# Performance work log

Measured on AMD Instinct MI355X. Metric: run time of the kernel, lower is better.

Reference implementation:

```python
import jax, jax.numpy as jnp
import numpy as np

IN_F = 4096      # in_features (d_model)
OUT_F = 16384    # out_features (4*d_model FFN)
N_TOK = 8192     # tokens = batch*seq
K = OUT_F // 2   # number of kept output rows (static for jit)


def setup_inputs() -> dict:
    key = jax.random.key(0)
    k1, k2, k3, k4 = jax.random.split(key, 4)
    data = jax.random.normal(k1, (N_TOK, IN_F), jnp.float32)
    weight = jax.random.normal(k2, (OUT_F, IN_F), jnp.float32) * 0.02
    bias = jax.random.normal(k3, (OUT_F,), jnp.float32) * 0.02
    # mask with exactly K ones at random positions (static count -> jit-safe)
    perm = jax.random.permutation(k4, OUT_F)
    mask = jnp.zeros((OUT_F,), jnp.int32).at[perm[:K]].set(1)
    return {"data": data, "weight": weight, "bias": bias, "mask": mask}


def reference(data, weight, bias, mask):
    # mask.nonzero()[0] -> selected output-feature indices (ascending, as torch)
    idx = jnp.nonzero(mask, size=K)[0]                 # [K]
    w_sel = jnp.take(weight, idx, axis=0)              # [K, IN_F] row gather
    b_sel = jnp.take(bias, idx, axis=0)                # [K]
    # F.linear: data @ w_sel^T + b_sel  -> [N_TOK, K]
    return jnp.einsum('ti,ki->tk', data, w_sel) + b_sel
```

## Files before the change

### kernel.cpp

```cpp
#include <hip/hip_runtime.h>
#include <hip/hip_bf16.h>

typedef __bf16 bf16_t;
typedef __attribute__((ext_vector_type(8))) __bf16 bf16x8;
typedef __attribute__((ext_vector_type(4))) float f32x4;

constexpr int IN_F  = 4096;
constexpr int OUT_F = 16384;
constexpr int N_TOK = 8192;
constexpr int KSEL  = 8192;
constexpr long A_ELEMS = (long)N_TOK * IN_F;

constexpr int BM = 256, BN = 256, BK = 32;
constexpr int NT = IN_F / BK;
constexpr int TILE_E = BM * BK;

#define GLOBAL_CAST(p) (const __attribute__((address_space(1))) void*)(p)
#define LDS_CAST(p)    (__attribute__((address_space(3))) void*)(p)

__global__ __launch_bounds__(1024) void build_idx_kernel(
    const int* __restrict__ mask, const float* __restrict__ bias,
    int* __restrict__ idx, float* __restrict__ bsel)
{
    const int t    = threadIdx.x;
    const int lane = t & 63;
    const int wave = t >> 6;
    const int base_i = t * 16;

    int m[16];
    const int4* mp = (const int4*)(mask + base_i);
#pragma unroll
    for (int v = 0; v < 4; ++v) {
        int4 q = mp[v];
        m[v*4+0] = q.x; m[v*4+1] = q.y; m[v*4+2] = q.z; m[v*4+3] = q.w;
    }
    int cnt = 0;
#pragma unroll
    for (int j = 0; j < 16; ++j) cnt += (m[j] != 0) ? 1 : 0;

    int incl = cnt;
#pragma unroll
    for (int d = 1; d < 64; d <<= 1) {
        int o = __shfl_up(incl, (unsigned)d);
        if (lane >= d) incl += o;
    }

    __shared__ int wsum[16];
    __shared__ int wbase[16];
    if (lane == 63) wsum[wave] = incl;
    __syncthreads();
    if (t == 0) {
        int s = 0;
        for (int w = 0; w < 16; ++w) { wbase[w] = s; s += wsum[w]; }
    }
    __syncthreads();

    int p = wbase[wave] + (incl - cnt);
#pragma unroll
    for (int j = 0; j < 16; ++j) {
        if (m[j]) {
            int i = base_i + j;
            idx[p]  = i;
            bsel[p] = bias[i];
            ++p;
        }
    }
}

__global__ __launch_bounds__(256) void convert_kernel(
    const float* __restrict__ A, const float* __restrict__ W,
    const int* __restrict__ idx,
    bf16_t* __restrict__ Ab, bf16_t* __restrict__ Wb)
{
    const long nvecA = A_ELEMS / 8;
    const long total = nvecA * 2;
    const long stride = (long)gridDim.x * blockDim.x;
    for (long v = (long)blockIdx.x * blockDim.x + threadIdx.x; v < total; v += stride) {
        const float4* src;
        bf16_t* dst;
        if (v < nvecA) {
            src = (const float4*)(A + v * 8);
            dst = Ab + v * 8;
        } else {
            long u = v - nvecA;
            int j = (int)(u >> 9);
            int k = (int)(u & 511) * 8;
            src = (const float4*)(W + (long)idx[j] * IN_F + k);
            dst = Wb + u * 8;
        }
        float4 x = src[0], y = src[1];
        bf16x8 o;
        o[0]=(bf16_t)x.x; o[1]=(bf16_t)x.y; o[2]=(bf16_t)x.z; o[3]=(bf16_t)x.w;
        o[4]=(bf16_t)y.x; o[5]=(bf16_t)y.y; o[6]=(bf16_t)y.z; o[7]=(bf16_t)y.w;
        *(bf16x8*)dst = o;
    }
}

__global__ __launch_bounds__(512, 2) void gemm8_kernel(
    const bf16_t* __restrict__ A, const bf16_t* __restrict__ B,
    const float* __restrict__ bsel, float* __restrict__ C)
{
    __shared__ __attribute__((aligned(16))) bf16_t As[4][TILE_E];
    __shared__ __attribute__((aligned(16))) bf16_t Bs[4][TILE_E];

    const int tid  = threadIdx.x;
    const int w    = tid >> 6;
    const int lane = tid & 63;
    const int wr   = w >> 2;
    const int wc   = w & 3;

    const int bid = blockIdx.x;
    const int swz = (bid & 7) * 128 + (bid >> 3);
    const int m0 = (swz & 31) * BM;
    const int n0 = (swz >> 5) * BN;

    const int prl = lane >> 3;
    const int sl  = (lane & 7) ^ prl;
    const int srow_off = 2 * prl + (sl >> 2);
    const int scol     = (sl & 3) * 8;
    const bf16_t* aS[2] = { A + (long)(m0 +       w * 16 + srow_off) * IN_F + scol,
                            A + (long)(m0 + 128 + w * 16 + srow_off) * IN_F + scol };
    const bf16_t* bS[2] = { B + (long)(n0 +       w * 16 + srow_off) * IN_F + scol,
                            B + (long)(n0 + 128 + w * 16 + srow_off) * IN_F + scol };

#define STAGE(buf, h, koff)                                                     \
    do {                                                                        \
        __builtin_amdgcn_global_load_lds(GLOBAL_CAST(aS[h] + (koff)),           \
            LDS_CAST(&As[buf][((h) * 128 + w * 16) * BK]), 16, 0, 0);           \
        __builtin_amdgcn_global_load_lds(GLOBAL_CAST(bS[h] + (koff)),           \
            LDS_CAST(&Bs[buf][((h) * 128 + w * 16) * BK]), 16, 0, 0);           \
    } while (0)

    f32x4 acc[8][4];
#pragma unroll
    for (int m = 0; m < 8; ++m)
#pragma unroll
        for (int n = 0; n < 4; ++n)
#pragma unroll
            for (int j = 0; j < 4; ++j) acc[m][n][j] = 0.f;

    const int fr    = lane & 15;
    const int kslot = lane >> 4;
    const int swz_e = (((((fr & 1) << 2) | kslot) ^ ((fr >> 1) & 7))) * 8;
    const int abase = (wr * 64 + (fr >> 1)) * 64 + swz_e;
    const int bbase = (wc * 32 + (fr >> 1)) * 64 + swz_e;

    STAGE(0, 0, 0);  STAGE(0, 1, 0);
    STAGE(1, 0, BK); STAGE(1, 1, BK);
    asm volatile("s_waitcnt vmcnt(4)" ::: "memory");
    __builtin_amdgcn_s_barrier();

    for (int t = 0; t < NT; ++t) {
        const int cb   = t & 3;
        const int sb   = (t + 2) & 3;
        const long koff = (long)(t + 2) * BK;
        const bool st  = (t + 2) < NT;

        bf16x8 af[8], bg[4];
#pragma unroll
        for (int m = 0; m < 4; ++m)
            af[m] = *(const bf16x8*)&As[cb][abase + m * 512];
#pragma unroll
        for (int n = 0; n < 4; ++n)
            bg[n] = *(const bf16x8*)&Bs[cb][bbase + n * 512];
        if (st) STAGE(sb, 0, koff);

        __builtin_amdgcn_s_setprio(1);
#pragma unroll
        for (int m = 0; m < 4; ++m)
#pragma unroll
            for (int n = 0; n < 4; ++n)
                acc[m][n] = __builtin_amdgcn_mfma_f32_16x16x32_bf16(
                    af[m], bg[n], acc[m][n], 0, 0, 0);
        __builtin_amdgcn_s_setprio(0);

#pragma unroll
        for (int m = 4; m < 8; ++m)
            af[m] = *(const bf16x8*)&As[cb][abase + m * 512];
        if (st) STAGE(sb, 1, koff);

        __builtin_amdgcn_s_setprio(1);
#pragma unroll
        for (int m = 4; m < 8; ++m)
#pragma unroll
            for (int n = 0; n < 4; ++n)
                acc[m][n] = __builtin_amdgcn_mfma_f32_16x16x32_bf16(
                    af[m], bg[n], acc[m][n], 0, 0, 0);
        __builtin_amdgcn_s_setprio(0);

        if (st) asm volatile("s_waitcnt vmcnt(4)" ::: "memory");
        else    asm volatile("s_waitcnt vmcnt(0)" ::: "memory");
        __builtin_amdgcn_s_barrier();
    }
#undef STAGE

    float b4[4];
#pragma unroll
    for (int n = 0; n < 4; ++n) b4[n] = bsel[n0 + wc * 64 + n * 16 + fr];

    const int rbase = m0 + wr * 128 + (lane >> 4) * 4;
#pragma unroll
    for (int m = 0; m < 8; ++m)
#pragma unroll
        for (int n = 0; n < 4; ++n) {
            const int col = n0 + wc * 64 + n * 16 + fr;
#pragma unroll
            for (int j = 0; j < 4; ++j)
                C[(long)(rbase + m * 16 + j) * KSEL + col] = acc[m][n][j] + b4[n];
        }
}

__global__ __launch_bounds__(256) void gemm_f32staged_kernel(
    const float* __restrict__ A, const float* __restrict__ W,
    const int* __restrict__ idx, const float* __restrict__ bsel,
    float* __restrict__ C)
{
    constexpr int FBM = 128, FBN = 128, BK2 = 32;
    __shared__ __attribute__((aligned(16))) float Asf[FBM * BK2];
    __shared__ __attribute__((aligned(16))) float Bsf[FBN * BK2];

    const int tid  = threadIdx.x;
    const int wave = tid >> 6;
    const int lane = tid & 63;
    const int wr   = wave >> 1;
    const int wc   = wave & 1;

    const int m0 = blockIdx.x * FBM;
    const int n0 = blockIdx.y * FBN;

    const int srow = lane >> 3;
    const int scol = (lane & 7) * 4;

    const float* aptr[4];
    const float* bptr[4];
#pragma unroll
    for (int i = 0; i < 4; ++i) {
        aptr[i] = A + (long)(m0 + wave * 32 + i * 8 + srow) * IN_F + scol;
        const int br = idx[n0 + wave * 32 + i * 8 + srow];
        bptr[i] = W + (long)br * IN_F + scol;
    }

    f32x4 acc[4][4];
#pragma unroll
    for (int m = 0; m < 4; ++m)
#pragma unroll
        for (int n = 0; n < 4; ++n)
#pragma unroll
            for (int j = 0; j < 4; ++j) acc[m][n][j] = 0.f;

    const int fr = lane & 15;
    const int fk = (lane >> 4) * 8;

    for (int k0 = 0; k0 < IN_F; k0 += BK2) {
#pragma unroll
        for (int i = 0; i < 4; ++i) {
            __builtin_amdgcn_global_load_lds(GLOBAL_CAST(aptr[i] + k0),
                LDS_CAST(&Asf[(wave * 32 + i * 8) * BK2]), 16, 0, 0);
            __builtin_amdgcn_global_load_lds(GLOBAL_CAST(bptr[i] + k0),
                LDS_CAST(&Bsf[(wave * 32 + i * 8) * BK2]), 16, 0, 0);
        }
        __syncthreads();

        bf16x8 af[4], bg[4];
#pragma unroll
        for (int m = 0; m < 4; ++m) {
            const float* p = &Asf[(wr * 64 + m * 16 + fr) * BK2 + fk];
            f32x4 x = *(const f32x4*)p, y = *(const f32x4*)(p + 4);
#pragma unroll
            for (int j = 0; j < 4; ++j) { af[m][j] = (bf16_t)x[j]; af[m][4+j] = (bf16_t)y[j]; }
        }
#pragma unroll
        for (int n = 0; n < 4; ++n) {
            const float* p = &Bsf[(wc * 64 + n * 16 + fr) * BK2 + fk];
            f32x4 x = *(const f32x4*)p, y = *(const f32x4*)(p + 4);
#pragma unroll
            for (int j = 0; j < 4; ++j) { bg[n][j] = (bf16_t)x[j]; bg[n][4+j] = (bf16_t)y[j]; }
        }
#pragma unroll
        for (int m = 0; m < 4; ++m)
#pragma unroll
            for (int n = 0; n < 4; ++n)
                acc[m][n] = __builtin_amdgcn_mfma_f32_16x16x32_bf16(
                    af[m], bg[n], acc[m][n], 0, 0, 0);
        __syncthreads();
    }

    float b4[4];
#pragma unroll
    for (int n = 0; n < 4; ++n) b4[n] = bsel[n0 + wc * 64 + n * 16 + fr];

    const int rbase = m0 + wr * 64 + (lane >> 4) * 4;
#pragma unroll
    for (int m = 0; m < 4; ++m)
#pragma unroll
        for (int n = 0; n < 4; ++n) {
            const int col = n0 + wc * 64 + n * 16 + fr;
#pragma unroll
            for (int j = 0; j < 4; ++j)
                C[(long)(rbase + m * 16 + j) * KSEL + col] = acc[m][n][j] + b4[n];
        }
}

extern "C" void kernel_launch(void* const* d_in, const int* in_sizes, int n_in,
                              void* d_out, int out_size, void* d_ws, size_t ws_size,
                              hipStream_t stream)
{
    const float* data   = (const float*)d_in[0];
    const float* weight = (const float*)d_in[1];
    const float* bias   = (const float*)d_in[2];
    const int*   mask   = (const int*)d_in[3];
    float*       out    = (float*)d_out;

    char* ws = (char*)d_ws;
    int*   idx  = (int*)ws;
    float* bsel = (float*)(ws + (KSEL * 4));
    bf16_t* Ab  = (bf16_t*)(ws + (KSEL * 8));
    bf16_t* Wb  = Ab + A_ELEMS;

    const size_t NEED = (size_t)KSEL * 8 + (size_t)A_ELEMS * 2 * 2;

    build_idx_kernel<<<1, 1024, 0, stream>>>(mask, bias, idx, bsel);

    if (ws_size >= NEED) {
        convert_kernel<<<2048, 256, 0, stream>>>(data, weight, idx, Ab, Wb);
        gemm8_kernel<<<1024, 512, 0, stream>>>(Ab, Wb, bsel, out);
    } else {
        dim3 grid(N_TOK / 128, KSEL / 128);
        gemm_f32staged_kernel<<<grid, 256, 0, stream>>>(data, weight, idx, bsel, out);
    }
}
```

Before: 816.8 us.

## Restructure bf16 GEMM main loop into 8-phase ping-pong schedule with BK=64

The bf16 GEMM's main loop is rebuilt around BK=64 K-tiles, split into A and B half-tiles held in double buffers. Each pair of K-tiles runs as eight phases that interleave LDS reads, async global-to-LDS loads and MFMA quadrants, separated by barriers and explicit lgkm/vm waits. This is meant to overlap memory traffic with matrix math more finely and halve the number of loop iterations. In exchange it adds many more barriers per iteration and a new LDS swizzle, so correctness and timing depend on the hand-tuned wait counts.

```diff
diff --git a/kernel.cpp b/kernel.cpp
--- a/kernel.cpp
+++ b/kernel.cpp
@@ -11,9 +11,9 @@
 constexpr int KSEL  = 8192;
 constexpr long A_ELEMS = (long)N_TOK * IN_F;
 
-constexpr int BM = 256, BN = 256, BK = 32;
+constexpr int BM = 256, BN = 256, BK = 64;
 constexpr int NT = IN_F / BK;
-constexpr int TILE_E = BM * BK;
+constexpr int HALF_E = 128 * BK;
 
 #define GLOBAL_CAST(p) (const __attribute__((address_space(1))) void*)(p)
 #define LDS_CAST(p)    (__attribute__((address_space(3))) void*)(p)
@@ -96,12 +96,12 @@
     }
 }
 
-__global__ __launch_bounds__(512, 2) void gemm8_kernel(
+__global__ __launch_bounds__(512, 2) void gemm8p_kernel(
     const bf16_t* __restrict__ A, const bf16_t* __restrict__ B,
     const float* __restrict__ bsel, float* __restrict__ C)
 {
-    __shared__ __attribute__((aligned(16))) bf16_t As[4][TILE_E];
-    __shared__ __attribute__((aligned(16))) bf16_t Bs[4][TILE_E];
+    __shared__ __attribute__((aligned(16))) bf16_t As[2][2][HALF_E];
+    __shared__ __attribute__((aligned(16))) bf16_t Bs[2][2][HALF_E];
 
     const int tid  = threadIdx.x;
     const int w    = tid >> 6;
@@ -114,22 +114,31 @@
     const int m0 = (swz & 31) * BM;
     const int n0 = (swz >> 5) * BN;
 
-    const int prl = lane >> 3;
-    const int sl  = (lane & 7) ^ prl;
-    const int srow_off = 2 * prl + (sl >> 2);
-    const int scol     = (sl & 3) * 8;
-    const bf16_t* aS[2] = { A + (long)(m0 +       w * 16 + srow_off) * IN_F + scol,
-                            A + (long)(m0 + 128 + w * 16 + srow_off) * IN_F + scol };
-    const bf16_t* bS[2] = { B + (long)(n0 +       w * 16 + srow_off) * IN_F + scol,
-                            B + (long)(n0 + 128 + w * 16 + srow_off) * IN_F + scol };
-
-#define STAGE(buf, h, koff)                                                     \
-    do {                                                                        \
-        __builtin_amdgcn_global_load_lds(GLOBAL_CAST(aS[h] + (koff)),           \
-            LDS_CAST(&As[buf][((h) * 128 + w * 16) * BK]), 16, 0, 0);           \
-        __builtin_amdgcn_global_load_lds(GLOBAL_CAST(bS[h] + (koff)),           \
-            LDS_CAST(&Bs[buf][((h) * 128 + w * 16) * BK]), 16, 0, 0);           \
-    } while (0)
+    const int pr  = lane >> 3;
+    const int csw = ((lane & 7) ^ pr) * 8;
+    const bf16_t* aSrc[2][2];
+    const bf16_t* bSrc[2][2];
+#pragma unroll
+    for (int h = 0; h < 2; ++h)
+#pragma unroll
+        for (int j = 0; j < 2; ++j) {
+            const int row = h * 128 + (w * 2 + j) * 8 + pr;
+            aSrc[h][j] = A + (long)(m0 + row) * IN_F + csw;
+            bSrc[h][j] = B + (long)(n0 + row) * IN_F + csw;
+        }
+
+#define STAGE_A(buf, h, tl) do {                                               \
+    __builtin_amdgcn_global_load_lds(GLOBAL_CAST(aSrc[h][0] + (long)(tl)*BK),  \
+        LDS_CAST(&As[buf][h][(w * 2 + 0) * 512]), 16, 0, 0);                   \
+    __builtin_amdgcn_global_load_lds(GLOBAL_CAST(aSrc[h][1] + (long)(tl)*BK),  \
+        LDS_CAST(&As[buf][h][(w * 2 + 1) * 512]), 16, 0, 0);                   \
+} while (0)
+#define STAGE_B(buf, h, tl) do {                                               \
+    __builtin_amdgcn_global_load_lds(GLOBAL_CAST(bSrc[h][0] + (long)(tl)*BK),  \
+        LDS_CAST(&Bs[buf][h][(w * 2 + 0) * 512]), 16, 0, 0);                   \
+    __builtin_amdgcn_global_load_lds(GLOBAL_CAST(bSrc[h][1] + (long)(tl)*BK),  \
+        LDS_CAST(&Bs[buf][h][(w * 2 + 1) * 512]), 16, 0, 0);                   \
+} while (0)
 
     f32x4 acc[8][4];
 #pragma unroll
@@ -141,64 +150,80 @@
 
     const int fr    = lane & 15;
     const int kslot = lane >> 4;
-    const int swz_e = (((((fr & 1) << 2) | kslot) ^ ((fr >> 1) & 7))) * 8;
-    const int abase = (wr * 64 + (fr >> 1)) * 64 + swz_e;
-    const int bbase = (wc * 32 + (fr >> 1)) * 64 + swz_e;
-
-    STAGE(0, 0, 0);  STAGE(0, 1, 0);
-    STAGE(1, 0, BK); STAGE(1, 1, BK);
-    asm volatile("s_waitcnt vmcnt(4)" ::: "memory");
-    __builtin_amdgcn_s_barrier();
-
-    for (int t = 0; t < NT; ++t) {
-        const int cb   = t & 3;
-        const int sb   = (t + 2) & 3;
-        const long koff = (long)(t + 2) * BK;
-        const bool st  = (t + 2) < NT;
-
-        bf16x8 af[8], bg[4];
-#pragma unroll
-        for (int m = 0; m < 4; ++m)
-            af[m] = *(const bf16x8*)&As[cb][abase + m * 512];
-#pragma unroll
-        for (int n = 0; n < 4; ++n)
-            bg[n] = *(const bf16x8*)&Bs[cb][bbase + n * 512];
-        if (st) STAGE(sb, 0, koff);
-
-        __builtin_amdgcn_s_setprio(1);
-#pragma unroll
-        for (int m = 0; m < 4; ++m)
-#pragma unroll
-            for (int n = 0; n < 4; ++n)
-                acc[m][n] = __builtin_amdgcn_mfma_f32_16x16x32_bf16(
-                    af[m], bg[n], acc[m][n], 0, 0, 0);
-        __builtin_amdgcn_s_setprio(0);
-
-#pragma unroll
-        for (int m = 4; m < 8; ++m)
-            af[m] = *(const bf16x8*)&As[cb][abase + m * 512];
-        if (st) STAGE(sb, 1, koff);
-
-        __builtin_amdgcn_s_setprio(1);
-#pragma unroll
-        for (int m = 4; m < 8; ++m)
-#pragma unroll
-            for (int n = 0; n < 4; ++n)
-                acc[m][n] = __builtin_amdgcn_mfma_f32_16x16x32_bf16(
-                    af[m], bg[n], acc[m][n], 0, 0, 0);
-        __builtin_amdgcn_s_setprio(0);
-
-        if (st) asm volatile("s_waitcnt vmcnt(4)" ::: "memory");
-        else    asm volatile("s_waitcnt vmcnt(0)" ::: "memory");
-        __builtin_amdgcn_s_barrier();
-    }
-#undef STAGE
+    const int sp0 = ((kslot     ^ (fr & 7)) << 3);
+    const int sp1 = (((4+kslot) ^ (fr & 7)) << 3);
+
+    bf16x8 af[4][2], bg[4][2];
+
+#define RDA(buf, mq) do {                                                      \
+    _Pragma("unroll") for (int mm = 0; mm < 4; ++mm) {                         \
+        const int r = ((mq) * 4 + mm) * 16 + fr;                               \
+        af[mm][0] = *(const bf16x8*)&As[buf][wr][r * 64 + sp0];                \
+        af[mm][1] = *(const bf16x8*)&As[buf][wr][r * 64 + sp1];                \
+    } } while (0)
+#define RDB(buf, nh) do {                                                      \
+    _Pragma("unroll") for (int nn = 0; nn < 2; ++nn) {                         \
+        const int r = (wc & 1) * 64 + ((nh) * 2 + nn) * 16 + fr;               \
+        bg[(nh)*2+nn][0] = *(const bf16x8*)&Bs[buf][wc >> 1][r * 64 + sp0];    \
+        bg[(nh)*2+nn][1] = *(const bf16x8*)&Bs[buf][wc >> 1][r * 64 + sp1];    \
+    } } while (0)
+#define MFMAQ(mq, nh) do {                                                     \
+    __builtin_amdgcn_s_setprio(1);                                             \
+    _Pragma("unroll") for (int mm = 0; mm < 4; ++mm)                           \
+    _Pragma("unroll") for (int nn = 0; nn < 2; ++nn) {                         \
+        const int m = (mq) * 4 + mm, n = (nh) * 2 + nn;                        \
+        acc[m][n] = __builtin_amdgcn_mfma_f32_16x16x32_bf16(                   \
+            af[mm][0], bg[n][0], acc[m][n], 0, 0, 0);                          \
+        acc[m][n] = __builtin_amdgcn_mfma_f32_16x16x32_bf16(                   \
+            af[mm][1], bg[n][1], acc[m][n], 0, 0, 0);                          \
+    }                                                                          \
+    __builtin_amdgcn_s_setprio(0); } while (0)
+#define BAR()   __builtin_amdgcn_s_barrier()
+#define LGKM0() do { asm volatile("s_waitcnt lgkmcnt(0)" ::: "memory");        \
+                     __builtin_amdgcn_sched_barrier(0); } while (0)
+#define VMC4()  asm volatile("s_waitcnt vmcnt(4)" ::: "memory")
+
+    STAGE_A(0, 0, 0); STAGE_A(0, 1, 0); STAGE_B(0, 0, 0); STAGE_B(0, 1, 0);
+    STAGE_B(1, 0, 1); STAGE_A(1, 0, 1);
+    VMC4(); BAR();
+
+    for (int I = 0; I < NT / 2; ++I) {
+        const int t = 2 * I, u = t + 1;
+        const bool s2 = (I < NT / 2 - 1);
+
+        RDA(0, 0); RDB(0, 0); STAGE_A(1, 1, u);
+        BAR(); LGKM0(); MFMAQ(0, 0); BAR();
+        RDB(0, 1); STAGE_B(1, 1, u);
+        BAR(); LGKM0(); MFMAQ(0, 1); BAR();
+        RDA(0, 1); if (s2) STAGE_B(0, 0, t + 2);
+        BAR(); LGKM0(); MFMAQ(1, 0); BAR();
+        if (s2) STAGE_A(0, 0, t + 2);
+        BAR(); MFMAQ(1, 1); VMC4(); BAR();
+        RDA(1, 0); RDB(1, 0); if (s2) STAGE_A(0, 1, t + 2);
+        BAR(); LGKM0(); MFMAQ(0, 0); BAR();
+        RDB(1, 1); if (s2) STAGE_B(0, 1, t + 2);
+        BAR(); LGKM0(); MFMAQ(0, 1); BAR();
+        RDA(1, 1); if (s2) STAGE_B(1, 0, u + 2);
+        BAR(); LGKM0(); MFMAQ(1, 0); BAR();
+        if (s2) STAGE_A(1, 0, u + 2);
+        BAR(); MFMAQ(1, 1); VMC4(); BAR();
+    }
+    asm volatile("s_waitcnt vmcnt(0)" ::: "memory");
+
+#undef STAGE_A
+#undef STAGE_B
+#undef RDA
+#undef RDB
+#undef MFMAQ
+#undef BAR
+#undef LGKM0
+#undef VMC4
 
     float b4[4];
 #pragma unroll
     for (int n = 0; n < 4; ++n) b4[n] = bsel[n0 + wc * 64 + n * 16 + fr];
 
-    const int rbase = m0 + wr * 128 + (lane >> 4) * 4;
+    const int rbase = m0 + wr * 128 + kslot * 4;
 #pragma unroll
     for (int m = 0; m < 8; ++m)
 #pragma unroll
@@ -222,8 +247,8 @@
     const int tid  = threadIdx.x;
     const int wave = tid >> 6;
     const int lane = tid & 63;
-    const int wr   = wave >> 1;
-    const int wc   = wave & 1;
+    const int wrf  = wave >> 1;
+    const int wcf  = wave & 1;
 
     const int m0 = blockIdx.x * FBM;
     const int n0 = blockIdx.y * FBN;
@@ -264,14 +289,14 @@
         bf16x8 af[4], bg[4];
 #pragma unroll
         for (int m = 0; m < 4; ++m) {
-            const float* p = &Asf[(wr * 64 + m * 16 + fr) * BK2 + fk];
+            const float* p = &Asf[(wrf * 64 + m * 16 + fr) * BK2 + fk];
             f32x4 x = *(const f32x4*)p, y = *(const f32x4*)(p + 4);
 #pragma unroll
             for (int j = 0; j < 4; ++j) { af[m][j] = (bf16_t)x[j]; af[m][4+j] = (bf16_t)y[j]; }
         }
 #pragma unroll
         for (int n = 0; n < 4; ++n) {
-            const float* p = &Bsf[(wc * 64 + n * 16 + fr) * BK2 + fk];
+            const float* p = &Bsf[(wcf * 64 + n * 16 + fr) * BK2 + fk];
             f32x4 x = *(const f32x4*)p, y = *(const f32x4*)(p + 4);
 #pragma unroll
             for (int j = 0; j < 4; ++j) { bg[n][j] = (bf16_t)x[j]; bg[n][4+j] = (bf16_t)y[j]; }
@@ -287,14 +312,14 @@
 
     float b4[4];
 #pragma unroll
-    for (int n = 0; n < 4; ++n) b4[n] = bsel[n0 + wc * 64 + n * 16 + fr];
-
-    const int rbase = m0 + wr * 64 + (lane >> 4) * 4;
+    for (int n = 0; n < 4; ++n) b4[n] = bsel[n0 + wcf * 64 + n * 16 + fr];
+
+    const int rbase = m0 + wrf * 64 + (lane >> 4) * 4;
 #pragma unroll
     for (int m = 0; m < 4; ++m)
 #pragma unroll
         for (int n = 0; n < 4; ++n) {
-            const int col = n0 + wc * 64 + n * 16 + fr;
+            const int col = n0 + wcf * 64 + n * 16 + fr;
 #pragma unroll
             for (int j = 0; j < 4; ++j)
                 C[(long)(rbase + m * 16 + j) * KSEL + col] = acc[m][n][j] + b4[n];
@@ -323,7 +348,7 @@
 
     if (ws_size >= NEED) {
         convert_kernel<<<2048, 256, 0, stream>>>(data, weight, idx, Ab, Wb);
-        gemm8_kernel<<<1024, 512, 0, stream>>>(Ab, Wb, bsel, out);
+        gemm8p_kernel<<<1024, 512, 0, stream>>>(Ab, Wb, bsel, out);
     } else {
         dim3 grid(N_TOK / 128, KSEL / 128);
         gemm_f32staged_kernel<<<grid, 256, 0, stream>>>(data, weight, idx, bsel, out);
```

New measurement: 730.5 us. 10.6% less time.
